# Optimization experiments

Measured on AMD Instinct MI355X. Metric: run time of the kernel, lower is better.

The kernel has to match this reference:

```python
import jax, jax.numpy as jnp
import numpy as np

B, L, I, H, C, E = 32, 2048, 512, 512, 512, 512
TEMP = 0.5
EPS = 1e-20


def setup_inputs() -> dict:
    key = jax.random.key(0)
    ks = jax.random.split(key, 8)
    s_in = 1.0 / np.sqrt(I)
    s_h = 1.0 / np.sqrt(H)
    s_c = 1.0 / np.sqrt(C)
    return {
        "inputs_BxLxI": jax.random.normal(ks[0], (B, L, I), dtype=jnp.float32),
        "W_h": jax.random.uniform(ks[1], (H, I), jnp.float32, -s_in, s_in),
        "b_h": jax.random.uniform(ks[2], (H,), jnp.float32, -s_in, s_in),
        "W_logits": jax.random.uniform(ks[3], (C, H), jnp.float32, -s_h, s_h),
        "b_logits": jax.random.uniform(ks[4], (C,), jnp.float32, -s_h, s_h),
        "codebook_CxE": jax.random.uniform(ks[5], (C, E), jnp.float32, -s_c, s_c),
        "u_noise": jax.random.uniform(ks[6], (B, L, C), dtype=jnp.float32),
        "testing": 0,
    }


def reference(inputs_BxLxI, W_h, b_h, W_logits, b_logits, codebook_CxE, u_noise, testing):
    # 1-layer MLP before quantization
    hiddens = jax.nn.relu(jnp.einsum('bli,hi->blh', inputs_BxLxI, W_h) + b_h)
    logits_BxLxC = jnp.einsum('blh,ch->blc', hiddens, W_logits) + b_logits

    if testing:
        ind = jnp.argmax(logits_BxLxC, axis=-1)
        onehot_BxLxC = jax.nn.one_hot(ind, C, dtype=logits_BxLxC.dtype)
    else:
        # gumbel-softmax with straight-through one-hot
        g = -jnp.log(-jnp.log(u_noise + EPS) + EPS)
        y = jax.nn.softmax((logits_BxLxC + g) / TEMP, axis=-1)
        ind = jnp.argmax(y, axis=-1)
        y_hard = jax.nn.one_hot(ind, C, dtype=y.dtype)
        onehot_BxLxC = jax.lax.stop_gradient(y_hard - y) + y

    # disguised embedding gather: onehot @ codebook
    codes_BxLxE = jnp.einsum('blc,ce->ble', onehot_BxLxC, codebook_CxE)
    return (logits_BxLxC, codes_BxLxE)
```

## Files before the change

### kernel.cpp

```cpp
#include <hip/hip_runtime.h>
#include <hip/hip_fp16.h>

typedef _Float16 h16;
typedef __attribute__((ext_vector_type(8))) _Float16 h16x8;
typedef __attribute__((ext_vector_type(4))) float f32x4;

#define KDIM 512
#define NDIM 512
#define LO_SCALE 4096.0f
#define LO_INV   0.000244140625f

__device__ __forceinline__ void gload16(const void* g, void* l) {
  __builtin_amdgcn_global_load_lds((const __attribute__((address_space(1))) void*)g,
                                   (__attribute__((address_space(3))) void*)l, 16, 0, 0);
}

#define WAITV(n) asm volatile("s_waitcnt vmcnt(" #n ")" ::: "memory")
#define WAITL0() asm volatile("s_waitcnt lgkmcnt(0)" ::: "memory")

__global__ void split_w(const float* __restrict__ Wh, const float* __restrict__ Wl,
                        h16* __restrict__ WhHi, h16* __restrict__ WhLo,
                        h16* __restrict__ WlHi, h16* __restrict__ WlLo) {
  int i = blockIdx.x * 256 + threadIdx.x;
  float a = Wh[i];
  h16 h = (h16)a;
  WhHi[i] = h; WhLo[i] = (h16)((a - (float)h) * LO_SCALE);
  a = Wl[i];
  h = (h16)a;
  WlHi[i] = h; WlLo[i] = (h16)((a - (float)h) * LO_SCALE);
}

template <int AF32, int EPI>
__launch_bounds__(256, 2)
__global__ void gemm4_k(const void* __restrict__ Aptr, const void* __restrict__ AptrLo,
                        const h16* __restrict__ BHi, const h16* __restrict__ BLo,
                        const float* __restrict__ bias,
                        float* __restrict__ Cf32,
                        h16* __restrict__ OHi, h16* __restrict__ OLo) {
  __shared__ __align__(16) char lds[65536];
  const int tid = threadIdx.x;
  const int wave = tid >> 6, lane = tid & 63;
  const int wg = (blockIdx.x & 7) * 256 + (blockIdx.x >> 3);
  const int bm = wg >> 2, bn = wg & 3;
  const int wm = wave >> 1, wn = wave & 1;
  const long arow0 = (long)bm * 128;
  const int brow0 = bn * 128;
  const int q = lane >> 4, rlo = lane & 15;

  f32x4 acc_hh[4][4] = {};
  f32x4 acc_mx[4][4] = {};

#define STAGE4(bufoff, kt)                                                    \
  {                                                                           \
    _Pragma("unroll")                                                         \
    for (int pass = 0; pass < 4; ++pass) {                \
      int p = pass * 4096 + wave * 1024 + lane * 16;                          \
      int row = p >> 7;                                                       \
      int gs = ((p >> 4) & 7) ^ (row & 7);                                    \
      if (AF32) {                                                             \
        long off = (arow0 + row) * 2048 + (kt) * 128 + gs * 16;               \
        gload16((const char*)Aptr + off,                                      \
                lds + (bufoff) + pass * 4096 + wave * 1024);                  \
      } else {                                                                \
        const char* sp = (gs & 4) ? (const char*)AptrLo : (const char*)Aptr;  \
        long off = (arow0 + row) * 1024 + (kt) * 64 + (gs & 3) * 16;          \
        gload16(sp + off, lds + (bufoff) + pass * 4096 + wave * 1024);        \
      }                                                                       \
    }                                                                         \
    _Pragma("unroll")                                                         \
    for (int pass = 0; pass < 4; ++pass) {                \
      int p = pass * 4096 + wave * 1024 + lane * 16;                          \
      int row = p >> 7;                                                       \
      int gs = ((p >> 4) & 7) ^ (row & 7);                                    \
      const char* sp = (gs & 4) ? (const char*)BLo : (const char*)BHi;        \
      long off = (long)(brow0 + row) * 1024 + (kt) * 64 + (gs & 3) * 16;      \
      gload16(sp + off, lds + (bufoff) + 16384 + pass * 4096 + wave * 1024);  \
    }                                                                         \
  }

  STAGE4(0, 0);
  STAGE4(32768, 1);

#pragma unroll
  for (int t = 0; t < 16; ++t) {
    if (t < 15) { WAITV(8); } else { WAITV(0); }
    __builtin_amdgcn_sched_barrier(0);
    __builtin_amdgcn_s_barrier();
    __builtin_amdgcn_sched_barrier(0);

    const char* buf = lds + (t & 1) * 32768;
    h16x8 ah[4], al[4], bh[4], bl[4];
#pragma unroll
    for (int i = 0; i < 4; ++i) {
      int row = wm * 64 + i * 16 + rlo;
      int sw = (row & 7) << 4;
      if (AF32) {
        f32x4 u0 = *(const f32x4*)(buf + row * 128 + ((q * 32) ^ sw));
        f32x4 u1 = *(const f32x4*)(buf + row * 128 + ((q * 32 + 16) ^ sw));
#pragma unroll
        for (int e = 0; e < 4; ++e) {
          h16 h = (h16)u0[e];
          ah[i][e] = h; al[i][e] = (h16)((u0[e] - (float)h) * LO_SCALE);
          h16 h2 = (h16)u1[e];
          ah[i][4 + e] = h2; al[i][4 + e] = (h16)((u1[e] - (float)h2) * LO_SCALE);
        }
      } else {
        ah[i] = *(const h16x8*)(buf + row * 128 + ((q * 16) ^ sw));
        al[i] = *(const h16x8*)(buf + row * 128 + ((q * 16 + 64) ^ sw));
      }
      int rb = wn * 64 + i * 16 + rlo;
      int swb = (rb & 7) << 4;
      bh[i] = *(const h16x8*)(buf + 16384 + rb * 128 + ((q * 16) ^ swb));
      bl[i] = *(const h16x8*)(buf + 16384 + rb * 128 + ((q * 16 + 64) ^ swb));
    }
#pragma unroll
    for (int i = 0; i < 4; ++i)
#pragma unroll
      for (int j = 0; j < 4; ++j)
        acc_hh[i][j] = __builtin_amdgcn_mfma_f32_16x16x32_f16(ah[i], bh[j], acc_hh[i][j], 0, 0, 0);
#pragma unroll
    for (int i = 0; i < 4; ++i)
#pragma unroll
      for (int j = 0; j < 4; ++j)
        acc_mx[i][j] = __builtin_amdgcn_mfma_f32_16x16x32_f16(ah[i], bl[j], acc_mx[i][j], 0, 0, 0);
#pragma unroll
    for (int i = 0; i < 4; ++i)
#pragma unroll
      for (int j = 0; j < 4; ++j)
        acc_mx[i][j] = __builtin_amdgcn_mfma_f32_16x16x32_f16(al[i], bh[j], acc_mx[i][j], 0, 0, 0);

    WAITL0();
    __builtin_amdgcn_sched_barrier(0);
    __builtin_amdgcn_s_barrier();
    __builtin_amdgcn_sched_barrier(0);
    if (t + 2 < 16) STAGE4((t & 1) * 32768, t + 2);
  }
#undef STAGE4

#pragma unroll
  for (int j = 0; j < 4; ++j) {
    int lcol = wn * 64 + j * 16 + rlo;
    float bv = bias[bn * 128 + lcol];
#pragma unroll
    for (int i = 0; i < 4; ++i)
#pragma unroll
      for (int r = 0; r < 4; ++r) {
        int lrow = wm * 64 + i * 16 + q * 4 + r;
        float v = acc_hh[i][j][r] + acc_mx[i][j][r] * LO_INV + bv;
        if (EPI == 0) {
          v = fmaxf(v, 0.0f);
          h16 h = (h16)v;
          h16 l = (h16)((v - (float)h) * LO_SCALE);
          unsigned uu = (unsigned)__builtin_bit_cast(unsigned short, h) |
                        ((unsigned)__builtin_bit_cast(unsigned short, l) << 16);
          *(unsigned*)(lds + lrow * 512 + lcol * 4) = uu;
        } else {
          *(float*)(lds + lrow * 512 + lcol * 4) = v;
        }
      }
  }
  __syncthreads();
#pragma unroll
  for (int pass = 0; pass < 16; ++pass) {
    int o = pass * 4096 + tid * 16;
    int lrow = o >> 9;
    int lcb = o & 511;
    if (EPI == 0) {
      uint4 d = *(const uint4*)(lds + o);
      uint2 hi, lo;
      hi.x = (d.x & 0xffffu) | (d.y << 16);
      hi.y = (d.z & 0xffffu) | (d.w << 16);
      lo.x = (d.x >> 16) | (d.y & 0xffff0000u);
      lo.y = (d.z >> 16) | (d.w & 0xffff0000u);
      long gb = (arow0 + lrow) * 1024 + bn * 256 + (lcb >> 1);
      *(uint2*)((char*)OHi + gb) = hi;
      *(uint2*)((char*)OLo + gb) = lo;
    } else {
      f32x4 d = *(const f32x4*)(lds + o);
      long gb = (arow0 + lrow) * 2048 + bn * 512 + lcb;
      *(f32x4*)((char*)Cf32 + gb) = d;
    }
  }
}

__global__ void k3_argmax_gather(const float* __restrict__ logits,
                                 const float* __restrict__ u,
                                 const float* __restrict__ cb,
                                 const int* __restrict__ testing,
                                 float* __restrict__ codes) {
  const int wave = threadIdx.x >> 6, lane = threadIdx.x & 63;
  const long row = (long)blockIdx.x * 4 + wave;
  const f32x4* lrow = (const f32x4*)(logits + row * 512);
  const f32x4* urow = (const f32x4*)(u + row * 512);
  const int test = *testing;

  float best = -3.4e38f;
  int bi = 0;
#pragma unroll
  for (int h = 0; h < 2; ++h) {
    int c4 = h * 64 + lane;
    f32x4 z = lrow[c4];
    if (!test) {
      f32x4 uu = urow[c4];
#pragma unroll
      for (int t = 0; t < 4; ++t)
        z[t] += -logf(-logf(uu[t] + 1e-20f) + 1e-20f);
    }
#pragma unroll
    for (int t = 0; t < 4; ++t) {
      int c = c4 * 4 + t;
      if (z[t] > best) { best = z[t]; bi = c; }
    }
  }
#pragma unroll
  for (int off = 32; off; off >>= 1) {
    float ob = __shfl_xor(best, off);
    int oi = __shfl_xor(bi, off);
    if (ob > best || (ob == best && oi < bi)) { best = ob; bi = oi; }
  }
  const f32x4* src = (const f32x4*)(cb + (long)bi * 512);
  f32x4* dst = (f32x4*)(codes + row * 512);
  dst[lane] = src[lane];
  dst[lane + 64] = src[lane + 64];
}

extern "C" void kernel_launch(void* const* d_in, const int* in_sizes, int n_in,
                              void* d_out, int out_size, void* d_ws, size_t ws_size,
                              hipStream_t stream) {
  const float* X = (const float*)d_in[0];
  const float* Wh = (const float*)d_in[1];
  const float* bh = (const float*)d_in[2];
  const float* Wl = (const float*)d_in[3];
  const float* bl = (const float*)d_in[4];
  const float* cb = (const float*)d_in[5];
  const float* u = (const float*)d_in[6];
  const int* testing = (const int*)d_in[7];

  float* logits = (float*)d_out;
  float* codes = logits + 33554432;
  h16* Hhi = (h16*)codes;
  h16* Hlo = Hhi + 33554432;

  h16* WhHi = (h16*)d_ws;
  h16* WhLo = WhHi + 262144;
  h16* WlHi = WhLo + 262144;
  h16* WlLo = WlHi + 262144;

  split_w<<<dim3(1024), dim3(256), 0, stream>>>(Wh, Wl, WhHi, WhLo, WlHi, WlLo);

  gemm4_k<1, 0><<<dim3(2048), dim3(256), 0, stream>>>(
      (const void*)X, nullptr, WhHi, WhLo, bh, nullptr, Hhi, Hlo);
  gemm4_k<0, 1><<<dim3(2048), dim3(256), 0, stream>>>(
      (const void*)Hhi, (const void*)Hlo, WlHi, WlLo, bl, logits, nullptr, nullptr);

  k3_argmax_gather<<<dim3(16384), dim3(256), 0, stream>>>(logits, u, cb, testing, codes);
}
```

Before: 301.0 us.

## Fuse Gumbel argmax into logits GEMM epilogue and pre-split X to fp16

```diff
diff --git a/kernel.cpp b/kernel.cpp
--- a/kernel.cpp
+++ b/kernel.cpp
@@ -3,6 +3,7 @@
 
 typedef _Float16 h16;
 typedef __attribute__((ext_vector_type(8))) _Float16 h16x8;
+typedef __attribute__((ext_vector_type(4))) _Float16 h16x4;
 typedef __attribute__((ext_vector_type(4))) float f32x4;
 
 #define KDIM 512
@@ -30,13 +31,29 @@
   WlHi[i] = h; WlLo[i] = (h16)((a - (float)h) * LO_SCALE);
 }
 
+__global__ void split_x(const f32x4* __restrict__ X, h16x4* __restrict__ XHi,
+                        h16x4* __restrict__ XLo) {
+  int i = blockIdx.x * 256 + threadIdx.x;
+  f32x4 a = X[i];
+  h16x4 hv, lv;
+#pragma unroll
+  for (int j = 0; j < 4; ++j) {
+    h16 h = (h16)a[j];
+    hv[j] = h;
+    lv[j] = (h16)((a[j] - (float)h) * LO_SCALE);
+  }
+  XHi[i] = hv; XLo[i] = lv;
+}
+
 template <int AF32, int EPI>
 __launch_bounds__(256, 2)
 __global__ void gemm4_k(const void* __restrict__ Aptr, const void* __restrict__ AptrLo,
                         const h16* __restrict__ BHi, const h16* __restrict__ BLo,
                         const float* __restrict__ bias,
                         float* __restrict__ Cf32,
-                        h16* __restrict__ OHi, h16* __restrict__ OLo) {
+                        h16* __restrict__ OHi, h16* __restrict__ OLo,
+                        const float* __restrict__ U, const int* __restrict__ testing,
+                        uint2* __restrict__ part) {
   __shared__ __align__(16) char lds[65536];
   const int tid = threadIdx.x;
   const int wave = tid >> 6, lane = tid & 63;
@@ -160,6 +177,7 @@
       }
   }
   __syncthreads();
+  const int test = (EPI == 1) ? *testing : 0;
 #pragma unroll
   for (int pass = 0; pass < 16; ++pass) {
     int o = pass * 4096 + tid * 16;
@@ -179,45 +197,49 @@
       f32x4 d = *(const f32x4*)(lds + o);
       long gb = (arow0 + lrow) * 2048 + bn * 512 + lcb;
       *(f32x4*)((char*)Cf32 + gb) = d;
+      f32x4 un = *(const f32x4*)((const char*)U + gb);
+      float m = -3.4e38f; int mi = 0;
+#pragma unroll
+      for (int e = 0; e < 4; ++e) {
+        float z = d[e];
+        if (!test) z += -logf(-logf(un[e] + 1e-20f) + 1e-20f);
+        int c = (lcb >> 2) + e;
+        if (z > m) { m = z; mi = c; }
+      }
+#pragma unroll
+      for (int off = 16; off; off >>= 1) {
+        float om = __shfl_xor(m, off);
+        int oi = __shfl_xor(mi, off);
+        if (om > m || (om == m && oi < mi)) { m = om; mi = oi; }
+      }
+      if ((tid & 31) == 0) {
+        uint2 pr;
+        pr.x = __builtin_bit_cast(unsigned, m);
+        pr.y = (unsigned)(bn * 128 + mi);
+        part[(arow0 + lrow) * 4 + bn] = pr;
+      }
     }
   }
 }
 
-__global__ void k3_argmax_gather(const float* __restrict__ logits,
-                                 const float* __restrict__ u,
-                                 const float* __restrict__ cb,
-                                 const int* __restrict__ testing,
-                                 float* __restrict__ codes) {
+__global__ void k3b_gather(const uint2* __restrict__ part,
+                           const float* __restrict__ cb,
+                           float* __restrict__ codes) {
   const int wave = threadIdx.x >> 6, lane = threadIdx.x & 63;
   const long row = (long)blockIdx.x * 4 + wave;
-  const f32x4* lrow = (const f32x4*)(logits + row * 512);
-  const f32x4* urow = (const f32x4*)(u + row * 512);
-  const int test = *testing;
-
-  float best = -3.4e38f;
-  int bi = 0;
-#pragma unroll
-  for (int h = 0; h < 2; ++h) {
-    int c4 = h * 64 + lane;
-    f32x4 z = lrow[c4];
-    if (!test) {
-      f32x4 uu = urow[c4];
-#pragma unroll
-      for (int t = 0; t < 4; ++t)
-        z[t] += -logf(-logf(uu[t] + 1e-20f) + 1e-20f);
-    }
-#pragma unroll
-    for (int t = 0; t < 4; ++t) {
-      int c = c4 * 4 + t;
-      if (z[t] > best) { best = z[t]; bi = c; }
-    }
-  }
-#pragma unroll
-  for (int off = 32; off; off >>= 1) {
-    float ob = __shfl_xor(best, off);
-    int oi = __shfl_xor(bi, off);
-    if (ob > best || (ob == best && oi < bi)) { best = ob; bi = oi; }
-  }
+  uint2 p0 = part[row * 4 + 0];
+  uint2 p1 = part[row * 4 + 1];
+  uint2 p2 = part[row * 4 + 2];
+  uint2 p3 = part[row * 4 + 3];
+  float best = __builtin_bit_cast(float, p0.x);
+  int bi = (int)p0.y;
+  float v = __builtin_bit_cast(float, p1.x);
+  if (v > best) { best = v; bi = (int)p1.y; }
+  v = __builtin_bit_cast(float, p2.x);
+  if (v > best) { best = v; bi = (int)p2.y; }
+  v = __builtin_bit_cast(float, p3.x);
+  if (v > best) { best = v; bi = (int)p3.y; }
+
   const f32x4* src = (const f32x4*)(cb + (long)bi * 512);
   f32x4* dst = (f32x4*)(codes + row * 512);
   dst[lane] = src[lane];
@@ -245,13 +267,26 @@
   h16* WhLo = WhHi + 262144;
   h16* WlHi = WhLo + 262144;
   h16* WlLo = WlHi + 262144;
+  uint2* part = (uint2*)((char*)d_ws + 2097152);
+  h16* Xhi = (h16*)((char*)d_ws + 4194304);
+  h16* Xlo = Xhi + 33554432;
+  const bool presplit = ws_size >= (size_t)4194304 + (size_t)134217728;
 
   split_w<<<dim3(1024), dim3(256), 0, stream>>>(Wh, Wl, WhHi, WhLo, WlHi, WlLo);
 
-  gemm4_k<1, 0><<<dim3(2048), dim3(256), 0, stream>>>(
-      (const void*)X, nullptr, WhHi, WhLo, bh, nullptr, Hhi, Hlo);
+  if (presplit) {
+    split_x<<<dim3(32768), dim3(256), 0, stream>>>((const f32x4*)X, (h16x4*)Xhi, (h16x4*)Xlo);
+    gemm4_k<0, 0><<<dim3(2048), dim3(256), 0, stream>>>(
+        (const void*)Xhi, (const void*)Xlo, WhHi, WhLo, bh, nullptr, Hhi, Hlo,
+        nullptr, nullptr, nullptr);
+  } else {
+    gemm4_k<1, 0><<<dim3(2048), dim3(256), 0, stream>>>(
+        (const void*)X, nullptr, WhHi, WhLo, bh, nullptr, Hhi, Hlo,
+        nullptr, nullptr, nullptr);
+  }
   gemm4_k<0, 1><<<dim3(2048), dim3(256), 0, stream>>>(
-      (const void*)Hhi, (const void*)Hlo, WlHi, WlLo, bl, logits, nullptr, nullptr);
-
-  k3_argmax_gather<<<dim3(16384), dim3(256), 0, stream>>>(logits, u, cb, testing, codes);
-}
+      (const void*)Hhi, (const void*)Hlo, WlHi, WlLo, bl, logits, nullptr, nullptr,
+      u, testing, part);
+
+  k3b_gather<<<dim3(16384), dim3(256), 0, stream>>>(part, cb, codes);
+}
```

After: 398.4 us. 32.4% more time.

## Split fp32 input to fp16 hi/lo once at LDS staging in first GEMM

Applied to the files above, without the earlier changes.

```diff
diff --git a/kernel.cpp b/kernel.cpp
--- a/kernel.cpp
+++ b/kernel.cpp
@@ -3,6 +3,7 @@
 
 typedef _Float16 h16;
 typedef __attribute__((ext_vector_type(8))) _Float16 h16x8;
+typedef __attribute__((ext_vector_type(4))) _Float16 h16x4;
 typedef __attribute__((ext_vector_type(4))) float f32x4;
 
 #define KDIM 512
@@ -17,6 +18,7 @@
 
 #define WAITV(n) asm volatile("s_waitcnt vmcnt(" #n ")" ::: "memory")
 #define WAITL0() asm volatile("s_waitcnt lgkmcnt(0)" ::: "memory")
+#define SB() __builtin_amdgcn_sched_barrier(0)
 
 __global__ void split_w(const float* __restrict__ Wh, const float* __restrict__ Wl,
                         h16* __restrict__ WhHi, h16* __restrict__ WhLo,
@@ -28,6 +30,162 @@
   a = Wl[i];
   h = (h16)a;
   WlHi[i] = h; WlLo[i] = (h16)((a - (float)h) * LO_SCALE);
+}
+
+__launch_bounds__(256, 2)
+__global__ void gemm5_k(const float* __restrict__ X,
+                        const h16* __restrict__ BHi, const h16* __restrict__ BLo,
+                        const float* __restrict__ bias,
+                        h16* __restrict__ OHi, h16* __restrict__ OLo) {
+  __shared__ __align__(16) char lds[65536];
+  const int tid = threadIdx.x;
+  const int wave = tid >> 6, lane = tid & 63;
+  const int wg = (blockIdx.x & 7) * 256 + (blockIdx.x >> 3);
+  const int bm = wg >> 2, bn = wg & 3;
+  const int wm = wave >> 1, wn = wave & 1;
+  const long arow0 = (long)bm * 128;
+  const int brow0 = bn * 128;
+  const int q = lane >> 4, rlo = lane & 15;
+
+  f32x4 acc_hh[4][4] = {};
+  f32x4 acc_mx[4][4] = {};
+  f32x4 areg[2][4];
+
+  auto aload = [&](f32x4 (&ar)[4], int kt) {
+#pragma unroll
+    for (int i = 0; i < 4; ++i) {
+      int so = i * 4096 + tid * 16;
+      int r = so >> 7, cbyte = so & 127;
+      ar[i] = *(const f32x4*)((const char*)X + (arow0 + r) * 2048 + (long)kt * 128 + cbyte);
+    }
+  };
+  auto awrite = [&](f32x4 (&ar)[4], int bufoff) {
+#pragma unroll
+    for (int i = 0; i < 4; ++i) {
+      int so = i * 4096 + tid * 16;
+      int r = so >> 7;
+      int jb = (tid & 7) * 8;
+      int sw = (r & 7) << 4;
+      f32x4 a = ar[i];
+      h16x4 hv, lv;
+#pragma unroll
+      for (int e = 0; e < 4; ++e) {
+        h16 h = (h16)a[e];
+        hv[e] = h;
+        lv[e] = (h16)((a[e] - (float)h) * LO_SCALE);
+      }
+      *(h16x4*)(lds + bufoff + r * 128 + (jb ^ sw)) = hv;
+      *(h16x4*)(lds + bufoff + r * 128 + ((jb + 64) ^ sw)) = lv;
+    }
+  };
+  auto bgld = [&](int bufoff, int kt) {
+#pragma unroll
+    for (int pass = 0; pass < 4; ++pass) {
+      int p = pass * 4096 + wave * 1024 + lane * 16;
+      int row = p >> 7;
+      int gs = ((p >> 4) & 7) ^ (row & 7);
+      const char* sp = (gs & 4) ? (const char*)BLo : (const char*)BHi;
+      long off = (long)(brow0 + row) * 1024 + (long)kt * 64 + (gs & 3) * 16;
+      gload16(sp + off, lds + bufoff + 16384 + pass * 4096 + wave * 1024);
+    }
+  };
+
+  aload(areg[0], 0);
+  aload(areg[1], 1);
+  WAITV(4);
+  awrite(areg[0], 0);
+  bgld(0, 0);
+  WAITV(4);
+  awrite(areg[1], 32768);
+  aload(areg[0], 2);
+  bgld(32768, 1);
+  WAITL0();
+
+#pragma unroll
+  for (int t = 0; t < 16; ++t) {
+    if (t <= 13) { WAITV(8); } else if (t == 14) { WAITV(4); } else { WAITV(0); }
+    SB();
+    __builtin_amdgcn_s_barrier();
+    SB();
+
+    const char* buf = lds + (t & 1) * 32768;
+    h16x8 ah[4], al[4], bh[4], bl[4];
+#pragma unroll
+    for (int i = 0; i < 4; ++i) {
+      int row = wm * 64 + i * 16 + rlo;
+      int sw = (row & 7) << 4;
+      ah[i] = *(const h16x8*)(buf + row * 128 + ((q * 16) ^ sw));
+      al[i] = *(const h16x8*)(buf + row * 128 + ((q * 16 + 64) ^ sw));
+      int rb = wn * 64 + i * 16 + rlo;
+      int swb = (rb & 7) << 4;
+      bh[i] = *(const h16x8*)(buf + 16384 + rb * 128 + ((q * 16) ^ swb));
+      bl[i] = *(const h16x8*)(buf + 16384 + rb * 128 + ((q * 16 + 64) ^ swb));
+    }
+#pragma unroll
+    for (int i = 0; i < 4; ++i)
+#pragma unroll
+      for (int j = 0; j < 4; ++j)
+        acc_hh[i][j] = __builtin_amdgcn_mfma_f32_16x16x32_f16(ah[i], bh[j], acc_hh[i][j], 0, 0, 0);
+#pragma unroll
+    for (int i = 0; i < 4; ++i)
+#pragma unroll
+      for (int j = 0; j < 4; ++j)
+        acc_mx[i][j] = __builtin_amdgcn_mfma_f32_16x16x32_f16(ah[i], bl[j], acc_mx[i][j], 0, 0, 0);
+#pragma unroll
+    for (int i = 0; i < 4; ++i)
+#pragma unroll
+      for (int j = 0; j < 4; ++j)
+        acc_mx[i][j] = __builtin_amdgcn_mfma_f32_16x16x32_f16(al[i], bh[j], acc_mx[i][j], 0, 0, 0);
+
+    WAITL0();
+    SB();
+    __builtin_amdgcn_s_barrier();
+    SB();
+    if (t <= 12) {
+      aload(areg[(t + 3) & 1], t + 3);
+      WAITV(8);
+      awrite(areg[(t + 2) & 1], (t & 1) * 32768);
+      bgld((t & 1) * 32768, t + 2);
+    } else if (t == 13) {
+      WAITV(4);
+      awrite(areg[1], 32768);
+      bgld(32768, 15);
+    }
+  }
+
+#pragma unroll
+  for (int j = 0; j < 4; ++j) {
+    int lcol = wn * 64 + j * 16 + rlo;
+    float bv = bias[bn * 128 + lcol];
+#pragma unroll
+    for (int i = 0; i < 4; ++i)
+#pragma unroll
+      for (int r = 0; r < 4; ++r) {
+        int lrow = wm * 64 + i * 16 + q * 4 + r;
+        float v = fmaxf(acc_hh[i][j][r] + acc_mx[i][j][r] * LO_INV + bv, 0.0f);
+        h16 h = (h16)v;
+        h16 l = (h16)((v - (float)h) * LO_SCALE);
+        unsigned uu = (unsigned)__builtin_bit_cast(unsigned short, h) |
+                      ((unsigned)__builtin_bit_cast(unsigned short, l) << 16);
+        *(unsigned*)(lds + lrow * 512 + lcol * 4) = uu;
+      }
+  }
+  __syncthreads();
+#pragma unroll
+  for (int pass = 0; pass < 16; ++pass) {
+    int o = pass * 4096 + tid * 16;
+    int lrow = o >> 9;
+    int lcb = o & 511;
+    uint4 d = *(const uint4*)(lds + o);
+    uint2 hi, lo;
+    hi.x = (d.x & 0xffffu) | (d.y << 16);
+    hi.y = (d.z & 0xffffu) | (d.w << 16);
+    lo.x = (d.x >> 16) | (d.y & 0xffff0000u);
+    lo.y = (d.z >> 16) | (d.w & 0xffff0000u);
+    long gb = (arow0 + lrow) * 1024 + bn * 256 + (lcb >> 1);
+    *(uint2*)((char*)OHi + gb) = hi;
+    *(uint2*)((char*)OLo + gb) = lo;
+  }
 }
 
 template <int AF32, int EPI>
@@ -53,22 +211,16 @@
 #define STAGE4(bufoff, kt)                                                    \
   {                                                                           \
     _Pragma("unroll")                                                         \
-    for (int pass = 0; pass < 4; ++pass) {                \
+    for (int pass = 0; pass < 4; ++pass) {                                    \
       int p = pass * 4096 + wave * 1024 + lane * 16;                          \
       int row = p >> 7;                                                       \
       int gs = ((p >> 4) & 7) ^ (row & 7);                                    \
-      if (AF32) {                                                             \
-        long off = (arow0 + row) * 2048 + (kt) * 128 + gs * 16;               \
-        gload16((const char*)Aptr + off,                                      \
-                lds + (bufoff) + pass * 4096 + wave * 1024);                  \
-      } else {                                                                \
-        const char* sp = (gs & 4) ? (const char*)AptrLo : (const char*)Aptr;  \
-        long off = (arow0 + row) * 1024 + (kt) * 64 + (gs & 3) * 16;          \
-        gload16(sp + off, lds + (bufoff) + pass * 4096 + wave * 1024);        \
-      }                                                                       \
+      const char* sp = (gs & 4) ? (const char*)AptrLo : (const char*)Aptr;    \
+      long off = (arow0 + row) * 1024 + (kt) * 64 + (gs & 3) * 16;            \
+      gload16(sp + off, lds + (bufoff) + pass * 4096 + wave * 1024);          \
     }                                                                         \
     _Pragma("unroll")                                                         \
-    for (int pass = 0; pass < 4; ++pass) {                \
+    for (int pass = 0; pass < 4; ++pass) {                                    \
       int p = pass * 4096 + wave * 1024 + lane * 16;                          \
       int row = p >> 7;                                                       \
       int gs = ((p >> 4) & 7) ^ (row & 7);                                    \
@@ -84,9 +236,9 @@
 #pragma unroll
   for (int t = 0; t < 16; ++t) {
     if (t < 15) { WAITV(8); } else { WAITV(0); }
-    __builtin_amdgcn_sched_barrier(0);
+    SB();
     __builtin_amdgcn_s_barrier();
-    __builtin_amdgcn_sched_barrier(0);
+    SB();
 
     const char* buf = lds + (t & 1) * 32768;
     h16x8 ah[4], al[4], bh[4], bl[4];
@@ -94,20 +246,8 @@
     for (int i = 0; i < 4; ++i) {
       int row = wm * 64 + i * 16 + rlo;
       int sw = (row & 7) << 4;
-      if (AF32) {
-        f32x4 u0 = *(const f32x4*)(buf + row * 128 + ((q * 32) ^ sw));
-        f32x4 u1 = *(const f32x4*)(buf + row * 128 + ((q * 32 + 16) ^ sw));
-#pragma unroll
-        for (int e = 0; e < 4; ++e) {
-          h16 h = (h16)u0[e];
-          ah[i][e] = h; al[i][e] = (h16)((u0[e] - (float)h) * LO_SCALE);
-          h16 h2 = (h16)u1[e];
-          ah[i][4 + e] = h2; al[i][4 + e] = (h16)((u1[e] - (float)h2) * LO_SCALE);
-        }
-      } else {
-        ah[i] = *(const h16x8*)(buf + row * 128 + ((q * 16) ^ sw));
-        al[i] = *(const h16x8*)(buf + row * 128 + ((q * 16 + 64) ^ sw));
-      }
+      ah[i] = *(const h16x8*)(buf + row * 128 + ((q * 16) ^ sw));
+      al[i] = *(const h16x8*)(buf + row * 128 + ((q * 16 + 64) ^ sw));
       int rb = wn * 64 + i * 16 + rlo;
       int swb = (rb & 7) << 4;
       bh[i] = *(const h16x8*)(buf + 16384 + rb * 128 + ((q * 16) ^ swb));
@@ -130,9 +270,9 @@
         acc_mx[i][j] = __builtin_amdgcn_mfma_f32_16x16x32_f16(al[i], bh[j], acc_mx[i][j], 0, 0, 0);
 
     WAITL0();
-    __builtin_amdgcn_sched_barrier(0);
+    SB();
     __builtin_amdgcn_s_barrier();
-    __builtin_amdgcn_sched_barrier(0);
+    SB();
     if (t + 2 < 16) STAGE4((t & 1) * 32768, t + 2);
   }
 #undef STAGE4
@@ -248,8 +388,8 @@
 
   split_w<<<dim3(1024), dim3(256), 0, stream>>>(Wh, Wl, WhHi, WhLo, WlHi, WlLo);
 
-  gemm4_k<1, 0><<<dim3(2048), dim3(256), 0, stream>>>(
-      (const void*)X, nullptr, WhHi, WhLo, bh, nullptr, Hhi, Hlo);
+  gemm5_k<<<dim3(2048), dim3(256), 0, stream>>>(X, WhHi, WhLo, bh, Hhi, Hlo);
+
   gemm4_k<0, 1><<<dim3(2048), dim3(256), 0, stream>>>(
       (const void*)Hhi, (const void*)Hlo, WlHi, WlLo, bl, logits, nullptr, nullptr);
 
```

Result: no change. 298.5 us (-0.8%).

## Use 256x128 tiles with 8 waves and register-staged fp32 A split

Applied to the files above, without the earlier changes.

```diff
diff --git a/kernel.cpp b/kernel.cpp
--- a/kernel.cpp
+++ b/kernel.cpp
@@ -17,6 +17,7 @@
 
 #define WAITV(n) asm volatile("s_waitcnt vmcnt(" #n ")" ::: "memory")
 #define WAITL0() asm volatile("s_waitcnt lgkmcnt(0)" ::: "memory")
+#define SB() __builtin_amdgcn_sched_barrier(0)
 
 __global__ void split_w(const float* __restrict__ Wh, const float* __restrict__ Wl,
                         h16* __restrict__ WhHi, h16* __restrict__ WhLo,
@@ -31,88 +32,119 @@
 }
 
 template <int AF32, int EPI>
-__launch_bounds__(256, 2)
-__global__ void gemm4_k(const void* __restrict__ Aptr, const void* __restrict__ AptrLo,
+__launch_bounds__(512, 1)
+__global__ void gemm9_k(const void* __restrict__ Aptr, const void* __restrict__ AptrLo,
                         const h16* __restrict__ BHi, const h16* __restrict__ BLo,
                         const float* __restrict__ bias,
                         float* __restrict__ Cf32,
                         h16* __restrict__ OHi, h16* __restrict__ OLo) {
-  __shared__ __align__(16) char lds[65536];
+  __shared__ __align__(16) char lds[131072];
   const int tid = threadIdx.x;
   const int wave = tid >> 6, lane = tid & 63;
-  const int wg = (blockIdx.x & 7) * 256 + (blockIdx.x >> 3);
+  const int wm = wave >> 1, wn = wave & 1;
+  const int wg = (blockIdx.x & 7) * 128 + (blockIdx.x >> 3);
   const int bm = wg >> 2, bn = wg & 3;
-  const int wm = wave >> 1, wn = wave & 1;
-  const long arow0 = (long)bm * 128;
+  const long arow0 = (long)bm * 256;
   const int brow0 = bn * 128;
   const int q = lane >> 4, rlo = lane & 15;
 
   f32x4 acc_hh[4][4] = {};
   f32x4 acc_mx[4][4] = {};
-
-#define STAGE4(bufoff, kt)                                                    \
-  {                                                                           \
-    _Pragma("unroll")                                                         \
-    for (int pass = 0; pass < 4; ++pass) {                \
-      int p = pass * 4096 + wave * 1024 + lane * 16;                          \
-      int row = p >> 7;                                                       \
-      int gs = ((p >> 4) & 7) ^ (row & 7);                                    \
-      if (AF32) {                                                             \
-        long off = (arow0 + row) * 2048 + (kt) * 128 + gs * 16;               \
-        gload16((const char*)Aptr + off,                                      \
-                lds + (bufoff) + pass * 4096 + wave * 1024);                  \
-      } else {                                                                \
-        const char* sp = (gs & 4) ? (const char*)AptrLo : (const char*)Aptr;  \
-        long off = (arow0 + row) * 1024 + (kt) * 64 + (gs & 3) * 16;          \
-        gload16(sp + off, lds + (bufoff) + pass * 4096 + wave * 1024);        \
-      }                                                                       \
-    }                                                                         \
-    _Pragma("unroll")                                                         \
-    for (int pass = 0; pass < 4; ++pass) {                \
-      int p = pass * 4096 + wave * 1024 + lane * 16;                          \
-      int row = p >> 7;                                                       \
-      int gs = ((p >> 4) & 7) ^ (row & 7);                                    \
-      const char* sp = (gs & 4) ? (const char*)BLo : (const char*)BHi;        \
-      long off = (long)(brow0 + row) * 1024 + (kt) * 64 + (gs & 3) * 16;      \
-      gload16(sp + off, lds + (bufoff) + 16384 + pass * 4096 + wave * 1024);  \
-    }                                                                         \
-  }
-
-  STAGE4(0, 0);
-  STAGE4(32768, 1);
+  f32x4 areg[2][4];
+
+  const int axrow = tid >> 1;
+  const int akoff = (tid & 1) * 64;
+  const int asw = (axrow & 7) << 4;
+
+  auto aload = [&](f32x4 (&ar)[4], int kt) {
+    const char* base = (const char*)Aptr + (arow0 + axrow) * 2048 + (long)kt * 128 + akoff;
+#pragma unroll
+    for (int i = 0; i < 4; ++i) ar[i] = *(const f32x4*)(base + i * 16);
+  };
+  auto awrite = [&](const f32x4 (&ar)[4], char* buf) {
+    h16x8 hv[2], lv[2];
+#pragma unroll
+    for (int p = 0; p < 4; ++p)
+#pragma unroll
+      for (int e = 0; e < 4; ++e) {
+        float a = ar[p][e];
+        h16 h = (h16)a;
+        hv[p >> 1][(p & 1) * 4 + e] = h;
+        lv[p >> 1][(p & 1) * 4 + e] = (h16)((a - (float)h) * LO_SCALE);
+      }
+    int jb = (tid & 1) * 32;
+#pragma unroll
+    for (int p = 0; p < 2; ++p) {
+      *(h16x8*)(buf + axrow * 128 + ((jb + p * 16) ^ asw)) = hv[p];
+      *(h16x8*)(buf + axrow * 128 + ((jb + p * 16 + 64) ^ asw)) = lv[p];
+    }
+  };
+  auto agld = [&](char* buf, int kt) {
+#pragma unroll
+    for (int pass = 0; pass < 4; ++pass) {
+      int p = pass * 8192 + wave * 1024 + lane * 16;
+      int row = p >> 7;
+      int gs = ((p >> 4) & 7) ^ (row & 7);
+      const char* sp = (gs & 4) ? (const char*)AptrLo : (const char*)Aptr;
+      long off = (arow0 + row) * 1024 + (long)kt * 64 + (gs & 3) * 16;
+      gload16(sp + off, buf + pass * 8192 + wave * 1024);
+    }
+  };
+  auto bgld = [&](char* buf, int kt) {
+#pragma unroll
+    for (int pass = 0; pass < 2; ++pass) {
+      int p = pass * 8192 + wave * 1024 + lane * 16;
+      int row = p >> 7;
+      int gs = ((p >> 4) & 7) ^ (row & 7);
+      const char* sp = (gs & 4) ? (const char*)BLo : (const char*)BHi;
+      long off = (long)(brow0 + row) * 1024 + (long)kt * 64 + (gs & 3) * 16;
+      gload16(sp + off, buf + 32768 + pass * 8192 + wave * 1024);
+    }
+  };
+
+  if (AF32) {
+    aload(areg[0], 0);
+    aload(areg[1], 1);
+    WAITV(4);
+    awrite(areg[0], lds);
+    bgld(lds, 0);
+    WAITV(2);
+    awrite(areg[1], lds + 49152);
+    aload(areg[0], 2);
+    bgld(lds + 49152, 1);
+    WAITL0();
+  } else {
+    agld(lds, 0); bgld(lds, 0);
+    agld(lds + 49152, 1); bgld(lds + 49152, 1);
+  }
 
 #pragma unroll
   for (int t = 0; t < 16; ++t) {
-    if (t < 15) { WAITV(8); } else { WAITV(0); }
-    __builtin_amdgcn_sched_barrier(0);
+    if (AF32) {
+      if (t <= 13) { WAITV(6); } else if (t == 14) { WAITV(2); } else { WAITV(0); }
+    } else {
+      if (t <= 14) { WAITV(6); } else { WAITV(0); }
+    }
+    SB();
     __builtin_amdgcn_s_barrier();
-    __builtin_amdgcn_sched_barrier(0);
-
-    const char* buf = lds + (t & 1) * 32768;
+    SB();
+
+    if (AF32 && t <= 12) aload(areg[(t + 3) & 1], t + 3);
+
+    char* buf = lds + (t & 1) * 49152;
     h16x8 ah[4], al[4], bh[4], bl[4];
 #pragma unroll
     for (int i = 0; i < 4; ++i) {
       int row = wm * 64 + i * 16 + rlo;
       int sw = (row & 7) << 4;
-      if (AF32) {
-        f32x4 u0 = *(const f32x4*)(buf + row * 128 + ((q * 32) ^ sw));
-        f32x4 u1 = *(const f32x4*)(buf + row * 128 + ((q * 32 + 16) ^ sw));
-#pragma unroll
-        for (int e = 0; e < 4; ++e) {
-          h16 h = (h16)u0[e];
-          ah[i][e] = h; al[i][e] = (h16)((u0[e] - (float)h) * LO_SCALE);
-          h16 h2 = (h16)u1[e];
-          ah[i][4 + e] = h2; al[i][4 + e] = (h16)((u1[e] - (float)h2) * LO_SCALE);
-        }
-      } else {
-        ah[i] = *(const h16x8*)(buf + row * 128 + ((q * 16) ^ sw));
-        al[i] = *(const h16x8*)(buf + row * 128 + ((q * 16 + 64) ^ sw));
-      }
+      ah[i] = *(const h16x8*)(buf + row * 128 + ((q * 16) ^ sw));
+      al[i] = *(const h16x8*)(buf + row * 128 + ((q * 16 + 64) ^ sw));
       int rb = wn * 64 + i * 16 + rlo;
       int swb = (rb & 7) << 4;
-      bh[i] = *(const h16x8*)(buf + 16384 + rb * 128 + ((q * 16) ^ swb));
-      bl[i] = *(const h16x8*)(buf + 16384 + rb * 128 + ((q * 16 + 64) ^ swb));
-    }
+      bh[i] = *(const h16x8*)(buf + 32768 + rb * 128 + ((q * 16) ^ swb));
+      bl[i] = *(const h16x8*)(buf + 32768 + rb * 128 + ((q * 16 + 64) ^ swb));
+    }
+    __builtin_amdgcn_s_setprio(1);
 #pragma unroll
     for (int i = 0; i < 4; ++i)
 #pragma unroll
@@ -128,14 +160,26 @@
 #pragma unroll
       for (int j = 0; j < 4; ++j)
         acc_mx[i][j] = __builtin_amdgcn_mfma_f32_16x16x32_f16(al[i], bh[j], acc_mx[i][j], 0, 0, 0);
+    __builtin_amdgcn_s_setprio(0);
 
     WAITL0();
-    __builtin_amdgcn_sched_barrier(0);
+    SB();
     __builtin_amdgcn_s_barrier();
-    __builtin_amdgcn_sched_barrier(0);
-    if (t + 2 < 16) STAGE4((t & 1) * 32768, t + 2);
-  }
-#undef STAGE4
+    SB();
+    if (AF32) {
+      if (t <= 12) {
+        WAITV(6);
+        awrite(areg[(t + 2) & 1], lds + (t & 1) * 49152);
+        bgld(lds + (t & 1) * 49152, t + 2);
+      } else if (t == 13) {
+        WAITV(2);
+        awrite(areg[1], lds + 49152);
+        bgld(lds + 49152, 15);
+      }
+    } else {
+      if (t + 2 < 16) { agld(lds + (t & 1) * 49152, t + 2); bgld(lds + (t & 1) * 49152, t + 2); }
+    }
+  }
 
 #pragma unroll
   for (int j = 0; j < 4; ++j) {
@@ -162,7 +206,7 @@
   __syncthreads();
 #pragma unroll
   for (int pass = 0; pass < 16; ++pass) {
-    int o = pass * 4096 + tid * 16;
+    int o = pass * 8192 + tid * 16;
     int lrow = o >> 9;
     int lcb = o & 511;
     if (EPI == 0) {
@@ -248,9 +292,10 @@
 
   split_w<<<dim3(1024), dim3(256), 0, stream>>>(Wh, Wl, WhHi, WhLo, WlHi, WlLo);
 
-  gemm4_k<1, 0><<<dim3(2048), dim3(256), 0, stream>>>(
+  gemm9_k<1, 0><<<dim3(1024), dim3(512), 0, stream>>>(
       (const void*)X, nullptr, WhHi, WhLo, bh, nullptr, Hhi, Hlo);
-  gemm4_k<0, 1><<<dim3(2048), dim3(256), 0, stream>>>(
+
+  gemm9_k<0, 1><<<dim3(1024), dim3(512), 0, stream>>>(
       (const void*)Hhi, (const void*)Hlo, WlHi, WlLo, bl, logits, nullptr, nullptr);
 
   k3_argmax_gather<<<dim3(16384), dim3(256), 0, stream>>>(logits, u, cb, testing, codes);
```

Result: slower. 316.8 us (+5.3%).
